# Kernel tuning notes

Measured on AMD Instinct MI355X. Metric: run time of the kernel, lower is better.

Reference implementation:

```python
import jax, jax.numpy as jnp
import numpy as np

D_MODEL = 1024
NUM_HEADS = 16
D_K = D_MODEL // NUM_HEADS
THETA = 10000.0
SEQ = 4096
BATCH = 1


def _rope(x, pos):
    # x: [..., S, d_k]; pos: [S]
    inv_freq = 1.0 / (THETA ** (jnp.arange(0, D_K, 2, dtype=jnp.float32) / D_K))  # [d_k/2]
    freqs = pos.astype(jnp.float32)[:, None] * inv_freq[None, :]  # [S, d_k/2]
    cos = jnp.cos(freqs)
    sin = jnp.sin(freqs)
    x_even = x[..., ::2]
    x_odd = x[..., 1::2]
    out1 = cos * x_even - sin * x_odd
    out2 = sin * x_even + cos * x_odd
    # interleave: stack on new last axis then flatten (matches torch.stack(...,-1).flatten(-2))
    out = jnp.stack([out1, out2], axis=-1).reshape(x.shape)
    return out


def setup_inputs() -> dict:
    key = jax.random.key(0)
    ks = jax.random.split(key, 5)
    std = (2.0 / (D_MODEL + D_MODEL)) ** 0.5
    x = jax.random.normal(ks[0], (BATCH, SEQ, D_MODEL), dtype=jnp.float32)
    wq = jax.random.normal(ks[1], (D_MODEL, D_MODEL), dtype=jnp.float32) * std
    wk = jax.random.normal(ks[2], (D_MODEL, D_MODEL), dtype=jnp.float32) * std
    wv = jax.random.normal(ks[3], (D_MODEL, D_MODEL), dtype=jnp.float32) * std
    wo = jax.random.normal(ks[4], (D_MODEL, D_MODEL), dtype=jnp.float32) * std
    return {"x": x, "wq": wq, "wk": wk, "wv": wv, "wo": wo}


def reference(x, wq, wk, wv, wo):
    b, s, d = x.shape
    # projections: y = x @ W.T  (weight stored [out, in])
    q = jnp.einsum('bsd,od->bso', x, wq)
    k = jnp.einsum('bsd,od->bso', x, wk)
    v = jnp.einsum('bsd,od->bso', x, wv)
    # split heads -> [b, h, s, d_k]
    q = q.reshape(b, s, NUM_HEADS, D_K).transpose(0, 2, 1, 3)
    k = k.reshape(b, s, NUM_HEADS, D_K).transpose(0, 2, 1, 3)
    v = v.reshape(b, s, NUM_HEADS, D_K).transpose(0, 2, 1, 3)
    pos = jnp.arange(s)
    q = _rope(q, pos)
    k = _rope(k, pos)
    scores = jnp.einsum('bhqd,bhkd->bhqk', q, k) / (D_K ** 0.5)
    causal = jnp.tril(jnp.ones((s, s), dtype=bool))
    scores = jnp.where(causal, scores, -jnp.inf)
    attn = jax.nn.softmax(scores, axis=-1)
    out = jnp.einsum('bhqk,bhkd->bhqd', attn, v)
    out = out.transpose(0, 2, 1, 3).reshape(b, s, d)
    out = jnp.einsum('bsd,od->bso', out, wo)
    return out
```

## Files before the change

kernel.cpp:

```cpp
#include <hip/hip_runtime.h>
#include <math.h>

#define SEQ    4096
#define DMODEL 1024
#define NHEADS 16
#define DK     64

typedef unsigned short u16;
typedef short bh8 __attribute__((ext_vector_type(8)));
typedef float f4  __attribute__((ext_vector_type(4)));
typedef float f16v __attribute__((ext_vector_type(16)));

__device__ __forceinline__ u16 f2b(float f) {
    union { float f; unsigned u; } v; v.f = f;
    unsigned u = v.u;
    return (u16)((u + 0x7FFFu + ((u >> 16) & 1u)) >> 16);
}
__device__ __forceinline__ unsigned pk2(float a, float b) {
    union { float f; unsigned u; } ua, ub; ua.f = a; ub.f = b;
    return (ua.u >> 16) | (ub.u & 0xFFFF0000u);
}

__global__ void cvt_all_kernel(const float* __restrict__ x,
                               const float* __restrict__ wq, const float* __restrict__ wk,
                               const float* __restrict__ wv, const float* __restrict__ wo,
                               u16* __restrict__ xb, u16* __restrict__ wb)
{
    const int NX = SEQ * DMODEL / 8;
    const int NW = DMODEL * DMODEL / 8;
    int i = blockIdx.x * blockDim.x + threadIdx.x;
    if (i >= NX + 4 * NW) return;
    const float* src; u16* dst; int j;
    if (i < NX) { src = x; dst = xb; j = i; }
    else {
        int k = i - NX;
        int wsel = k >> 17;
        j = k & (NW - 1);
        src = (wsel == 0) ? wq : (wsel == 1) ? wk : (wsel == 2) ? wv : wo;
        dst = wb + (size_t)wsel * DMODEL * DMODEL;
    }
    const float4* p = (const float4*)src + (size_t)j * 2;
    float4 a = p[0], b = p[1];
    __align__(16) u16 r[8] = { f2b(a.x), f2b(a.y), f2b(a.z), f2b(a.w),
                               f2b(b.x), f2b(b.y), f2b(b.z), f2b(b.w) };
    *(uint4*)(dst + (size_t)j * 8) = *(const uint4*)r;
}

template<int MODE>
__global__ __launch_bounds__(256) void gemm_bt(
    const u16* __restrict__ A, const u16* __restrict__ B,
    void* __restrict__ out, u16* __restrict__ Qh, u16* __restrict__ Kh,
    u16* __restrict__ Vt, int M, int N, int K)
{
    constexpr int BN  = (MODE == 0) ? 64 : 128;
    constexpr int NJ  = BN / 32;
    constexpr int ASZ = 128 * 32;
    constexpr int BSZ = BN * 32;

    __shared__ __align__(16) u16 sh[2][ASZ + BSZ];

    const int t    = threadIdx.x;
    const int w    = t >> 6, lane = t & 63;
    const int quad = lane >> 4, l16 = lane & 15;
    const int wm   = w >> 1,  wn  = w & 1;
    const int m0   = blockIdx.y * 128, n0 = blockIdx.x * BN;
    const int lr   = lane >> 2;
    const int lc   = (lane & 3) * 8;
    const int c0   = 2 * w, c1 = 2 * w + 1;

    f4 acc[4][NJ];
#pragma unroll
    for (int i = 0; i < 4; ++i)
#pragma unroll
        for (int j = 0; j < NJ; ++j) { f4 z = {0.f,0.f,0.f,0.f}; acc[i][j] = z; }

    const size_t aofs0 = (size_t)(m0 + c0 * 16 + lr) * K + lc;
    const size_t aofs1 = (size_t)(m0 + c1 * 16 + lr) * K + lc;
    size_t bofs0 = 0, bofs1 = 0;
    if (MODE == 0) {
        bofs0 = (size_t)(n0 + w * 16 + lr) * K + lc;
    } else {
        const int br0 = c0 * 16 + lr, br1 = c1 * 16 + lr;
        const int p0 = (br0 & 64) | ((br0 & 15) << 2) | ((br0 >> 4) & 3);
        const int p1 = (br1 & 64) | ((br1 & 15) << 2) | ((br1 >> 4) & 3);
        bofs0 = (size_t)(n0 + p0) * K + lc;
        bofs1 = (size_t)(n0 + p1) * K + lc;
    }

#define GLD(src_, dst_)                                                        \
    __builtin_amdgcn_global_load_lds(                                          \
        (const __attribute__((address_space(1))) unsigned int*)(src_),         \
        (__attribute__((address_space(3))) unsigned int*)(dst_), 16, 0, 0)

#define STAGE(buf_, k0_) do {                                                  \
    GLD(A + aofs0 + (k0_), &sh[buf_][c0 * 512]);                               \
    GLD(A + aofs1 + (k0_), &sh[buf_][c1 * 512]);                               \
    if (MODE == 0) {                                                           \
        GLD(B + bofs0 + (k0_), &sh[buf_][ASZ + w * 512]);                      \
    } else {                                                                   \
        GLD(B + bofs0 + (k0_), &sh[buf_][ASZ + c0 * 512]);                     \
        GLD(B + bofs1 + (k0_), &sh[buf_][ASZ + c1 * 512]);                     \
    }                                                                          \
} while (0)

    STAGE(0, 0);
    __syncthreads();

    int b = 0;
    for (int k0 = 0; k0 < K; k0 += 32) {
        if (k0 + 32 < K) STAGE(b ^ 1, k0 + 32);

        const u16* As_ = &sh[b][0];
        const u16* Bs_ = &sh[b][ASZ];
        bh8 af[4], bf_[NJ];
#pragma unroll
        for (int i = 0; i < 4; ++i)
            af[i] = *(const bh8*)&As_[(wm * 64 + i * 16 + l16) * 32 + quad * 8];
#pragma unroll
        for (int j = 0; j < NJ; ++j)
            bf_[j] = *(const bh8*)&Bs_[(wn * (BN / 2) + j * 16 + l16) * 32 + quad * 8];
#pragma unroll
        for (int i = 0; i < 4; ++i)
#pragma unroll
            for (int j = 0; j < NJ; ++j)
                acc[i][j] = __builtin_amdgcn_mfma_f32_16x16x32_bf16(af[i], bf_[j], acc[i][j], 0, 0, 0);
        __syncthreads();
        b ^= 1;
    }

    if (MODE == 0) {
#pragma unroll
        for (int i = 0; i < 4; ++i) {
            const int row = m0 + wm * 64 + i * 16 + quad * 4;
#pragma unroll
            for (int j = 0; j < NJ; ++j) {
                const int col = n0 + wn * (BN / 2) + j * 16 + l16;
#pragma unroll
                for (int r = 0; r < 4; ++r)
                    ((float*)out)[(size_t)(row + r) * N + col] = acc[i][j][r];
            }
        }
    } else {
        const int sect = n0 >> 10;
        if (sect < 2) {
            const int hh = ((n0 & 1023) + wn * 64) >> 6;
            u16* dst = (sect == 0) ? Qh : Kh;
            const float qscl = (sect == 0) ? 0.18033688011112042f : 1.0f;
            const int dbase = l16 * 4;
            const float invfA = exp2f((float)(dbase)     * (-13.287712379549449f / 64.0f))
                                * 0.15915494309189535f;
            const float invfB = exp2f((float)(dbase + 2) * (-13.287712379549449f / 64.0f))
                                * 0.15915494309189535f;
#pragma unroll
            for (int i = 0; i < 4; ++i) {
                const int srow0 = m0 + wm * 64 + i * 16 + quad * 4;
#pragma unroll
                for (int r = 0; r < 4; ++r) {
                    const int srow = srow0 + r;
                    float revA = (float)srow * invfA;  revA -= floorf(revA);
                    float revB = (float)srow * invfB;  revB -= floorf(revB);
                    const float snA = __builtin_amdgcn_sinf(revA);
                    const float csA = __builtin_amdgcn_cosf(revA);
                    const float snB = __builtin_amdgcn_sinf(revB);
                    const float csB = __builtin_amdgcn_cosf(revB);
                    const float e0 = acc[i][0][r], o0 = acc[i][1][r];
                    const float e1 = acc[i][2][r], o1 = acc[i][3][r];
                    const float v0 = (csA * e0 - snA * o0) * qscl;
                    const float v1 = (snA * e0 + csA * o0) * qscl;
                    const float v2 = (csB * e1 - snB * o1) * qscl;
                    const float v3 = (snB * e1 + csB * o1) * qscl;
                    uint2 st;
                    st.x = (unsigned)f2b(v0) | ((unsigned)f2b(v1) << 16);
                    st.y = (unsigned)f2b(v2) | ((unsigned)f2b(v3) << 16);
                    *(uint2*)&dst[((size_t)hh * SEQ + srow) * DK + dbase] = st;
                }
            }
        } else {
            u16* scr = &sh[0][0];
            const int cfb = wn * 64 + l16 * 4;
            const int xv  = (l16 & 7) << 2;
            __syncthreads();
#pragma unroll
            for (int i = 0; i < 4; ++i) {
                const int s0 = wm * 64 + i * 16 + quad * 4;
                const int s8 = s0 >> 2;
#pragma unroll
                for (int j = 0; j < NJ; ++j) {
                    __align__(8) u16 pk[4];
#pragma unroll
                    for (int r = 0; r < 4; ++r) pk[r] = f2b(acc[i][j][r]);
                    *(unsigned long long*)&scr[(cfb + j) * 128 + (s8 ^ xv) * 4] =
                        *(const unsigned long long*)pk;
                }
            }
            __syncthreads();
            const int hh0 = (n0 & 1023) >> 6;
            const int sl  = t & 15;
#pragma unroll
            for (int jj = 0; jj < 8; ++jj) {
                const int cfull = jj * 16 + (t >> 4);
                const int hd    = hh0 + (cfull >> 6);
                const int dd    = cfull & 63;
                const int rxv   = ((cfull >> 2) & 7) << 2;
                bh8 vv = *(const bh8*)&scr[cfull * 128 + ((sl * 2) ^ rxv) * 4];
                *(bh8*)&Vt[((size_t)hd * DK + dd) * SEQ + m0 + sl * 8] = vv;
            }
        }
    }
#undef STAGE
#undef GLD
}

__global__ __launch_bounds__(512, 4) void attn_mfma_kernel(
    const u16* __restrict__ Qh, const u16* __restrict__ Kh,
    const u16* __restrict__ Vt, u16* __restrict__ ctx)
{
    __shared__ __align__(16) u16 smem[2][16384];

    const int id   = blockIdx.x;
    const int head = (id & 7) + 8 * ((id >> 3) & 1);
    const int bx   = id >> 4;

    const int t    = threadIdx.x;
    const int w    = t >> 6, lane = t & 63;
    const int qb   = w & 1, kb = w >> 1;
    const int l31  = lane & 31, hl = lane >> 5;
    const int r7   = l31 & 7;

    const u16* Kbase = Kh + (size_t)head * SEQ * DK;
    const u16* Vbase = Vt + (size_t)head * DK * SEQ;

    int kread[4];
#pragma unroll
    for (int c = 0; c < 4; ++c)
        kread[c] = (kb * 32 + l31) * 64 + (((c * 2 + hl) ^ r7) * 8);
    int vread[2][2];
#pragma unroll
    for (int db = 0; db < 2; ++db)
#pragma unroll
        for (int kc = 0; kc < 2; ++kc)
            vread[db][kc] = (db * 32 + l31) * 128
                          + (((kb * 4 + kc * 2 + hl) ^ r7) * 8);

    int koff[2], voff[2];
#pragma unroll
    for (int i = 0; i < 2; ++i) {
        const int krow = i * 64 + (t >> 3);
        koff[i] = krow * DK + (((t & 7) ^ (krow & 7)) * 8);
        const int vdr  = i * 32 + (t >> 4);
        voff[i] = vdr * SEQ + (((t & 15) ^ (vdr & 7)) * 8);
    }
    const int dstK = w * 512;
    const int dstV = 8192 + w * 512;

#define STAGE(buf_, kbase_) do {                                               \
    _Pragma("unroll")                                                          \
    for (int i_ = 0; i_ < 2; ++i_) {                                           \
        __builtin_amdgcn_global_load_lds(                                      \
            (const __attribute__((address_space(1))) unsigned int*)            \
                (Kbase + (size_t)(kbase_) * DK + koff[i_]),                    \
            (__attribute__((address_space(3))) unsigned int*)                  \
                &smem[buf_][i_ * 4096 + dstK], 16, 0, 0);                      \
        __builtin_amdgcn_global_load_lds(                                      \
            (const __attribute__((address_space(1))) unsigned int*)            \
                (Vbase + (kbase_) + voff[i_]),                                 \
            (__attribute__((address_space(3))) unsigned int*)                  \
                &smem[buf_][i_ * 4096 + dstV], 16, 0, 0);                      \
    }                                                                          \
} while (0)

    for (int part = 0; part < 2; ++part) {
        const int qt = part ? (63 - bx) : bx;
        const int q0 = qt * 64;
        const int nt = qt / 2 + 1;
        const int qg = q0 + qb * 32 + l31;

        bh8 qa[4];
        {
            const u16* qrow = Qh + ((size_t)head * SEQ + qg) * DK;
#pragma unroll
            for (int c = 0; c < 4; ++c)
                qa[c] = *(const bh8*)(qrow + c * 16 + hl * 8);
        }

        f16v o0 = {0,0,0,0,0,0,0,0,0,0,0,0,0,0,0,0};
        f16v o1 = {0,0,0,0,0,0,0,0,0,0,0,0,0,0,0,0};
        float lsum = 0.f;

        __syncthreads();
        STAGE(0, 0);
        __syncthreads();

        int b = 0;
        for (int kt = 0; kt < nt; ++kt) {
            const bool have_next = (kt + 1 < nt);
            if (have_next) STAGE(b ^ 1, (kt + 1) * 128);

            const int  kbase = kt * 128;
            const bool diag  = (kt == nt - 1);
            const bool skip  = diag && (kbase + kb * 32 > q0 + qb * 32 + 31);

            if (!skip) {
                f16v s = {0,0,0,0,0,0,0,0,0,0,0,0,0,0,0,0};
                __builtin_amdgcn_s_setprio(1);
#pragma unroll
                for (int c = 0; c < 4; ++c) {
                    bh8 kf = *(const bh8*)&smem[b][kread[c]];
                    s = __builtin_amdgcn_mfma_f32_32x32x16_bf16(kf, qa[c], s, 0, 0, 0);
                }
                __builtin_amdgcn_s_setprio(0);
                if (diag) {
#pragma unroll
                    for (int r = 0; r < 16; ++r) {
                        const int keyg = kbase + kb * 32 + (r & 3) + 8 * (r >> 2) + 4 * hl;
                        if (keyg > qg) s[r] = -1.0e30f;
                    }
                }
                float p[16];
#pragma unroll
                for (int r = 0; r < 16; ++r) { p[r] = exp2f(s[r]); lsum += p[r]; }

#pragma unroll
                for (int kc = 0; kc < 2; ++kc) {
                    unsigned A0 = pk2(p[kc*8+0], p[kc*8+1]);
                    unsigned A1 = pk2(p[kc*8+2], p[kc*8+3]);
                    unsigned A2 = pk2(p[kc*8+4], p[kc*8+5]);
                    unsigned A3 = pk2(p[kc*8+6], p[kc*8+7]);
                    asm volatile("v_permlane32_swap_b32 %0, %1" : "+v"(A0), "+v"(A2));
                    asm volatile("v_permlane32_swap_b32 %0, %1" : "+v"(A1), "+v"(A3));
                    union { unsigned u[4]; bh8 v; } pb;
                    pb.u[0] = A0; pb.u[1] = A1; pb.u[2] = A2; pb.u[3] = A3;
                    bh8 va0 = *(const bh8*)&smem[b][8192 + vread[0][kc]];
                    bh8 va1 = *(const bh8*)&smem[b][8192 + vread[1][kc]];
                    __builtin_amdgcn_s_setprio(1);
                    o0 = __builtin_amdgcn_mfma_f32_32x32x16_bf16(va0, pb.v, o0, 0, 0, 0);
                    o1 = __builtin_amdgcn_mfma_f32_32x32x16_bf16(va1, pb.v, o1, 0, 0, 0);
                    __builtin_amdgcn_s_setprio(0);
                }
            }

            if (have_next) { __syncthreads(); b ^= 1; }
        }

        lsum += __shfl_xor(lsum, 32);
        __syncthreads();
        float* scr = (float*)&smem[0][0];
        union { f16v v; f4 q[4]; } uo0, uo1;
        uo0.v = o0; uo1.v = o1;
        if (kb != 0) {
            float* rec = scr + (((kb - 1) * 2 + qb) * 64 + lane) * 33;
#pragma unroll
            for (int j = 0; j < 4; ++j) {
                *(f4*)(rec + j * 4)      = uo0.q[j];
                *(f4*)(rec + 16 + j * 4) = uo1.q[j];
            }
            rec[32] = lsum;
        }
        __syncthreads();
        if (kb == 0) {
#pragma unroll
            for (int jr = 0; jr < 3; ++jr) {
                const float* rec = scr + ((jr * 2 + qb) * 64 + lane) * 33;
#pragma unroll
                for (int j = 0; j < 4; ++j) {
                    f4 a = *(const f4*)(rec + j * 4);
                    f4 c = *(const f4*)(rec + 16 + j * 4);
#pragma unroll
                    for (int e = 0; e < 4; ++e) {
                        uo0.q[j][e] += a[e];
                        uo1.q[j][e] += c[e];
                    }
                }
                lsum += rec[32];
            }
            const float linv = 1.f / lsum;
            const size_t rowbase = (size_t)qg * DMODEL + head * DK;
#pragma unroll
            for (int a = 0; a < 4; ++a) {
                unsigned lo = (unsigned)f2b(uo0.q[a][0] * linv) | ((unsigned)f2b(uo0.q[a][1] * linv) << 16);
                unsigned hi = (unsigned)f2b(uo0.q[a][2] * linv) | ((unsigned)f2b(uo0.q[a][3] * linv) << 16);
                uint2 pkd; pkd.x = lo; pkd.y = hi;
                *(uint2*)&ctx[rowbase + a * 8 + 4 * hl] = pkd;
                lo = (unsigned)f2b(uo1.q[a][0] * linv) | ((unsigned)f2b(uo1.q[a][1] * linv) << 16);
                hi = (unsigned)f2b(uo1.q[a][2] * linv) | ((unsigned)f2b(uo1.q[a][3] * linv) << 16);
                pkd.x = lo; pkd.y = hi;
                *(uint2*)&ctx[rowbase + 32 + a * 8 + 4 * hl] = pkd;
            }
        }
    }
#undef STAGE
}

extern "C" void kernel_launch(void* const* d_in, const int* in_sizes, int n_in,
                              void* d_out, int out_size, void* d_ws, size_t ws_size,
                              hipStream_t stream)
{
    const float* x  = (const float*)d_in[0];
    const float* wq = (const float*)d_in[1];
    const float* wk = (const float*)d_in[2];
    const float* wv = (const float*)d_in[3];
    const float* wo = (const float*)d_in[4];
    float* out = (float*)d_out;

    char* ws = (char*)d_ws;
    const size_t MB = 1u << 20;
    u16* xb   = (u16*)(ws);
    u16* wqkv = (u16*)(ws + 8  * MB);
    u16* wob  = (u16*)(ws + 14 * MB);
    u16* Qh   = (u16*)(ws + 16 * MB);
    u16* Kh   = (u16*)(ws + 24 * MB);
    u16* Vtb  = (u16*)(ws + 32 * MB);
    u16* ctxb = (u16*)(ws + 40 * MB);

    const int NCVT = SEQ * DMODEL / 8 + 4 * (DMODEL * DMODEL / 8);
    cvt_all_kernel<<<NCVT / 256, 256, 0, stream>>>(x, wq, wk, wv, wo, xb, wqkv);

    dim3 gqkv(3 * DMODEL / 128, SEQ / 128);
    gemm_bt<2><<<gqkv, 256, 0, stream>>>(xb, wqkv, nullptr, Qh, Kh, Vtb,
                                         SEQ, 3 * DMODEL, DMODEL);

    attn_mfma_kernel<<<dim3(512), 512, 0, stream>>>(Qh, Kh, Vtb, ctxb);

    dim3 go(DMODEL / 64, SEQ / 128);
    gemm_bt<0><<<go, 256, 0, stream>>>(ctxb, wob, out, nullptr, nullptr, nullptr,
                                       SEQ, DMODEL, DMODEL);
}
```

Before: 204.1 us.

## Swizzle GEMM block order and use AMDGCN intrinsics in attention and RoPE

The GEMM launches switch to 1D grids with a grouped block index, so blocks working in the same column group of B run close together and reuse it in L2. Separately, exp2 and fract use the AMDGCN builtins, pk2 uses v_perm, and the first MFMA of the score tile takes a zero accumulator instead of a zeroed register vector. The padding stride of the attention reduction scratch changes from 33 to 36 floats, which aligns the f4 stores. These are several unrelated micro-optimizations plus a swizzle that assumes exact grid sizes; a dead pk2 computation that is immediately overwritten was also added.

```diff
diff --git a/kernel.cpp b/kernel.cpp
--- a/kernel.cpp
+++ b/kernel.cpp
@@ -16,9 +16,29 @@
     unsigned u = v.u;
     return (u16)((u + 0x7FFFu + ((u >> 16) & 1u)) >> 16);
 }
+__device__ __forceinline__ unsigned bits_of(float f) {
+    union { float f; unsigned u; } v; v.f = f; return v.u;
+}
 __device__ __forceinline__ unsigned pk2(float a, float b) {
-    union { float f; unsigned u; } ua, ub; ua.f = a; ub.f = b;
-    return (ua.u >> 16) | (ub.u & 0xFFFF0000u);
+#if __has_builtin(__builtin_amdgcn_perm)
+    return __builtin_amdgcn_perm(bits_of(b), bits_of(a), 0x07060302u);
+#else
+    return (bits_of(a) >> 16) | (bits_of(b) & 0xFFFF0000u);
+#endif
+}
+__device__ __forceinline__ float fexp2(float x) {
+#if __has_builtin(__builtin_amdgcn_exp2f)
+    return __builtin_amdgcn_exp2f(x);
+#else
+    return exp2f(x);
+#endif
+}
+__device__ __forceinline__ float ffract(float x) {
+#if __has_builtin(__builtin_amdgcn_fractf)
+    return __builtin_amdgcn_fractf(x);
+#else
+    return x - floorf(x);
+#endif
 }
 
 __global__ void cvt_all_kernel(const float* __restrict__ x,
@@ -59,11 +79,15 @@
 
     __shared__ __align__(16) u16 sh[2][ASZ + BSZ];
 
+    const int g    = blockIdx.x;
+    const int xt   = (g >> 8) * 8 + (g & 7);
+    const int yt   = (g & 255) >> 3;
+    const int m0   = yt * 128, n0 = xt * BN;
+
     const int t    = threadIdx.x;
     const int w    = t >> 6, lane = t & 63;
     const int quad = lane >> 4, l16 = lane & 15;
     const int wm   = w >> 1,  wn  = w & 1;
-    const int m0   = blockIdx.y * 128, n0 = blockIdx.x * BN;
     const int lr   = lane >> 2;
     const int lc   = (lane & 3) * 8;
     const int c0   = 2 * w, c1 = 2 * w + 1;
@@ -157,8 +181,8 @@
 #pragma unroll
                 for (int r = 0; r < 4; ++r) {
                     const int srow = srow0 + r;
-                    float revA = (float)srow * invfA;  revA -= floorf(revA);
-                    float revB = (float)srow * invfB;  revB -= floorf(revB);
+                    const float revA = ffract((float)srow * invfA);
+                    const float revB = ffract((float)srow * invfB);
                     const float snA = __builtin_amdgcn_sinf(revA);
                     const float csA = __builtin_amdgcn_cosf(revA);
                     const float snB = __builtin_amdgcn_sinf(revB);
@@ -252,6 +276,8 @@
     }
     const int dstK = w * 512;
     const int dstV = 8192 + w * 512;
+
+    const f16v z16 = {0,0,0,0,0,0,0,0,0,0,0,0,0,0,0,0};
 
 #define STAGE(buf_, kbase_) do {                                               \
     _Pragma("unroll")                                                          \
@@ -283,8 +309,8 @@
                 qa[c] = *(const bh8*)(qrow + c * 16 + hl * 8);
         }
 
-        f16v o0 = {0,0,0,0,0,0,0,0,0,0,0,0,0,0,0,0};
-        f16v o1 = {0,0,0,0,0,0,0,0,0,0,0,0,0,0,0,0};
+        f16v o0 = z16;
+        f16v o1 = z16;
         float lsum = 0.f;
 
         __syncthreads();
@@ -301,10 +327,11 @@
             const bool skip  = diag && (kbase + kb * 32 > q0 + qb * 32 + 31);
 
             if (!skip) {
-                f16v s = {0,0,0,0,0,0,0,0,0,0,0,0,0,0,0,0};
                 __builtin_amdgcn_s_setprio(1);
-#pragma unroll
-                for (int c = 0; c < 4; ++c) {
+                bh8 kf0 = *(const bh8*)&smem[b][kread[0]];
+                f16v s = __builtin_amdgcn_mfma_f32_32x32x16_bf16(kf0, qa[0], z16, 0, 0, 0);
+#pragma unroll
+                for (int c = 1; c < 4; ++c) {
                     bh8 kf = *(const bh8*)&smem[b][kread[c]];
                     s = __builtin_amdgcn_mfma_f32_32x32x16_bf16(kf, qa[c], s, 0, 0, 0);
                 }
@@ -318,7 +345,7 @@
                 }
                 float p[16];
 #pragma unroll
-                for (int r = 0; r < 16; ++r) { p[r] = exp2f(s[r]); lsum += p[r]; }
+                for (int r = 0; r < 16; ++r) { p[r] = fexp2(s[r]); lsum += p[r]; }
 
 #pragma unroll
                 for (int kc = 0; kc < 2; ++kc) {
@@ -348,7 +375,7 @@
         union { f16v v; f4 q[4]; } uo0, uo1;
         uo0.v = o0; uo1.v = o1;
         if (kb != 0) {
-            float* rec = scr + (((kb - 1) * 2 + qb) * 64 + lane) * 33;
+            float* rec = scr + (((kb - 1) * 2 + qb) * 64 + lane) * 36;
 #pragma unroll
             for (int j = 0; j < 4; ++j) {
                 *(f4*)(rec + j * 4)      = uo0.q[j];
@@ -360,7 +387,7 @@
         if (kb == 0) {
 #pragma unroll
             for (int jr = 0; jr < 3; ++jr) {
-                const float* rec = scr + ((jr * 2 + qb) * 64 + lane) * 33;
+                const float* rec = scr + ((jr * 2 + qb) * 64 + lane) * 36;
 #pragma unroll
                 for (int j = 0; j < 4; ++j) {
                     f4 a = *(const f4*)(rec + j * 4);
@@ -377,7 +404,9 @@
             const size_t rowbase = (size_t)qg * DMODEL + head * DK;
 #pragma unroll
             for (int a = 0; a < 4; ++a) {
-                unsigned lo = (unsigned)f2b(uo0.q[a][0] * linv) | ((unsigned)f2b(uo0.q[a][1] * linv) << 16);
+                unsigned lo = pk2(0.f, uo0.q[a][0] * linv) >> 16 |
+                              (pk2(0.f, uo0.q[a][1] * linv) & 0xFFFF0000u);
+                lo = (unsigned)f2b(uo0.q[a][0] * linv) | ((unsigned)f2b(uo0.q[a][1] * linv) << 16);
                 unsigned hi = (unsigned)f2b(uo0.q[a][2] * linv) | ((unsigned)f2b(uo0.q[a][3] * linv) << 16);
                 uint2 pkd; pkd.x = lo; pkd.y = hi;
                 *(uint2*)&ctx[rowbase + a * 8 + 4 * hl] = pkd;
@@ -415,13 +444,11 @@
     const int NCVT = SEQ * DMODEL / 8 + 4 * (DMODEL * DMODEL / 8);
     cvt_all_kernel<<<NCVT / 256, 256, 0, stream>>>(x, wq, wk, wv, wo, xb, wqkv);
 
-    dim3 gqkv(3 * DMODEL / 128, SEQ / 128);
-    gemm_bt<2><<<gqkv, 256, 0, stream>>>(xb, wqkv, nullptr, Qh, Kh, Vtb,
-                                         SEQ, 3 * DMODEL, DMODEL);
+    gemm_bt<2><<<dim3(768), 256, 0, stream>>>(xb, wqkv, nullptr, Qh, Kh, Vtb,
+                                              SEQ, 3 * DMODEL, DMODEL);
 
     attn_mfma_kernel<<<dim3(512), 512, 0, stream>>>(Qh, Kh, Vtb, ctxb);
 
-    dim3 go(DMODEL / 64, SEQ / 128);
-    gemm_bt<0><<<go, 256, 0, stream>>>(ctxb, wob, out, nullptr, nullptr, nullptr,
-                                       SEQ, DMODEL, DMODEL);
-}
+    gemm_bt<0><<<dim3(512), 256, 0, stream>>>(ctxb, wob, out, nullptr, nullptr, nullptr,
+                                              SEQ, DMODEL, DMODEL);
+}
```

Measured after the change: 182.1 us. 10.8% less time.
